# Kernel optimization log

Hardware: AMD Instinct MI355X
Metric: run time of the kernel (lower is better)

## Reference

```python
import jax, jax.numpy as jnp
import numpy as np

B, S, D, H = 2, 2048, 1024, 16
HD = D // H  # head_dim = 64

def setup_inputs() -> dict:
    key = jax.random.key(0)
    ks = jax.random.split(key, 6)
    sc = 0.02
    return {
        "x": jax.random.normal(ks[0], (B, S, D), dtype=jnp.float32),
        "Wq": jax.random.normal(ks[1], (D, D), dtype=jnp.float32) * sc,
        "Wk": jax.random.normal(ks[2], (D, D), dtype=jnp.float32) * sc,
        "Wv": jax.random.normal(ks[3], (D, D), dtype=jnp.float32) * sc,
        "Wo": jax.random.normal(ks[4], (D, D), dtype=jnp.float32) * sc,
        "bo": jnp.zeros((D,), dtype=jnp.float32),
    }

def reference(x, Wq, Wk, Wv, Wo, bo):
    b, s, d = x.shape
    # QKV projections (no bias, qkv_bias=False)
    q = (x @ Wq).reshape(b, s, H, HD).transpose(0, 2, 1, 3)  # [b,h,s,hd]
    k = (x @ Wk).reshape(b, s, H, HD).transpose(0, 2, 1, 3)
    v = (x @ Wv).reshape(b, s, H, HD).transpose(0, 2, 1, 3)
    scores = jnp.einsum("bhqd,bhkd->bhqk", q, k)  # [b,h,s,s]
    causal = jnp.triu(jnp.ones((s, s), dtype=bool), k=1)
    scores = jnp.where(causal, -jnp.inf, scores)
    # NOTE: source divides by keys.shape[-1]**0 / 5 == 1/5 -> scores / 5 (faithful)
    attn = jax.nn.softmax(scores / 5.0, axis=-1)
    ctx = jnp.einsum("bhqk,bhkd->bhqd", attn, v)  # [b,h,s,hd]
    ctx = ctx.transpose(0, 2, 1, 3).reshape(b, s, d)
    return ctx @ Wo + bo
```

## Files before the change

kernel.cpp:

```cpp
#include <hip/hip_runtime.h>
#include <math.h>

#define BB 2
#define SS 2048
#define DD 1024
#define HH 16
#define HD 64
#define MM (BB*SS)

typedef float  f32x4 __attribute__((ext_vector_type(4)));
typedef short  s16x8 __attribute__((ext_vector_type(8)));
typedef unsigned short u16;
typedef u16    u16x4 __attribute__((ext_vector_type(4)));
typedef unsigned int u32;
typedef u32    u32x2 __attribute__((ext_vector_type(2)));
typedef u32    u32x4 __attribute__((ext_vector_type(4)));

static __device__ __forceinline__ u16 f2bf(float f) {
    u32 u = __float_as_uint(f);
    u = (u + 0x7FFFu + ((u >> 16) & 1u)) >> 16;
    return (u16)u;
}

static __device__ __forceinline__ u32 cvtpk_bf16(float lo, float hi) {
    u32 r;
    asm("v_cvt_pk_bf16_f32 %0, %1, %2" : "=v"(r) : "v"(lo), "v"(hi));
    return r;
}

static __device__ __forceinline__ void gload16(const u16* g, void* l) {
    __builtin_amdgcn_global_load_lds((const __attribute__((address_space(1))) u32*)g,
                                     (__attribute__((address_space(3))) u32*)l, 16, 0, 0);
}

__global__ __launch_bounds__(256) void conv_x(const float* __restrict__ in,
                                              u16* __restrict__ outb) {
    int i = blockIdx.x * 256 + threadIdx.x;
    const f32x4* p = (const f32x4*)in;
    f32x4 a = p[i*2], b = p[i*2 + 1];
    u16x4 lo, hi;
    lo[0]=f2bf(a.x); lo[1]=f2bf(a.y); lo[2]=f2bf(a.z); lo[3]=f2bf(a.w);
    hi[0]=f2bf(b.x); hi[1]=f2bf(b.y); hi[2]=f2bf(b.z); hi[3]=f2bf(b.w);
    *(u16x4*)(outb + (size_t)i*8)     = lo;
    *(u16x4*)(outb + (size_t)i*8 + 4) = hi;
}

__global__ __launch_bounds__(256) void conv_wt(const float* __restrict__ W0,
                                               const float* __restrict__ W1,
                                               const float* __restrict__ W2,
                                               const float* __restrict__ W3,
                                               u16* __restrict__ WT) {
    const int z = blockIdx.z;
    const float* W = (z==0) ? W0 : (z==1) ? W1 : (z==2) ? W2 : W3;
    u16* dst = WT + (size_t)z * 1024 * 1024;
    __shared__ u16 tr[64][72];
    const int t = threadIdx.x;
    const int r0 = blockIdx.y * 64, c0 = blockIdx.x * 64;
    #pragma unroll
    for (int u = 0; u < 4; ++u) {
        int idx = u*256 + t;
        int r = idx >> 4, c4 = (idx & 15) * 4;
        f32x4 v = *(const f32x4*)(W + (size_t)(r0 + r)*1024 + c0 + c4);
        tr[c4+0][r] = f2bf(v.x);
        tr[c4+1][r] = f2bf(v.y);
        tr[c4+2][r] = f2bf(v.z);
        tr[c4+3][r] = f2bf(v.w);
    }
    __syncthreads();
    {
        int c = t >> 2, rq = (t & 3) * 16;
        u32x4 v0 = *(const u32x4*)&tr[c][rq];
        u32x4 v1 = *(const u32x4*)&tr[c][rq + 8];
        u16* op = dst + (size_t)(c0 + c)*1024 + r0 + rq;
        *(u32x4*)op       = v0;
        *(u32x4*)(op + 8) = v1;
    }
}

template<int EPI, int NJ>
__global__ __launch_bounds__(256) void mfma_gemm(const u16* __restrict__ A,
                                                 const u16* __restrict__ WT,
                                                 const float* __restrict__ bias,
                                                 u16* __restrict__ Qb,
                                                 u16* __restrict__ Kb,
                                                 u16* __restrict__ Vtb,
                                                 float* __restrict__ outF) {
    constexpr int BN  = NJ * 32;
    constexpr int ASZ = 16384;
    constexpr int BSZ = NJ * 4096;
    __shared__ u32x4 smemv[(2*(ASZ + BSZ))/16];
    char* smem = (char*)smemv;
    char* A0 = smem;
    char* B0 = smem + ASZ;
    char* A1 = smem + ASZ + BSZ;
    char* B1 = smem + 2*ASZ + BSZ;
    const int t   = threadIdx.x;
    const int w   = t >> 6;
    const int l   = t & 63;
    const int c15 = l & 15;
    const int g16 = ((l >> 4) & 3) << 4;
    const int mw  = w >> 1, nw = w & 1;
    const int brow = blockIdx.y * 128;
    const int bcol = blockIdx.x * BN;

    f32x4 acc[4][NJ] = {};

    const u16* Asrc = A  + (size_t)brow * DD;
    const u16* Bsrc = WT + (size_t)bcol * DD;

    auto stage = [&](int k0, char* Ab, char* Bb) {
        #pragma unroll
        for (int u = 0; u < 4; ++u) {
            int idx = u*256 + t;
            int row = idx >> 3;
            int cb  = (idx & 7) << 4;
            int off = (cb ^ ((row & 7) << 4)) >> 1;
            gload16(Asrc + (size_t)row*DD + k0 + off, Ab + ((idx - l) << 4));
        }
        #pragma unroll
        for (int u = 0; u < NJ; ++u) {
            int idx = u*256 + t;
            int row = idx >> 3;
            int cb  = (idx & 7) << 4;
            int off = (cb ^ ((row & 7) << 4)) >> 1;
            gload16(Bsrc + (size_t)row*DD + k0 + off, Bb + ((idx - l) << 4));
        }
    };

    auto compute = [&](char* Ab, char* Bb) {
        s16x8 af[4][2], bf[NJ][2];
        #pragma unroll
        for (int mi = 0; mi < 4; ++mi) {
            int row = mw*64 + mi*16 + c15;
            int sw  = (row & 7) << 4;
            af[mi][0] = *(const s16x8*)(Ab + row*128 + ((g16)      ^ sw));
            af[mi][1] = *(const s16x8*)(Ab + row*128 + ((64 + g16) ^ sw));
        }
        #pragma unroll
        for (int nj = 0; nj < NJ; ++nj) {
            int row = nw*(NJ*16) + nj*16 + c15;
            int sw  = (row & 7) << 4;
            bf[nj][0] = *(const s16x8*)(Bb + row*128 + ((g16)      ^ sw));
            bf[nj][1] = *(const s16x8*)(Bb + row*128 + ((64 + g16) ^ sw));
        }
        #pragma unroll
        for (int c = 0; c < 2; ++c)
            #pragma unroll
            for (int mi = 0; mi < 4; ++mi)
                #pragma unroll
                for (int nj = 0; nj < NJ; ++nj)
                    acc[mi][nj] = __builtin_amdgcn_mfma_f32_16x16x32_bf16(
                        af[mi][c], bf[nj][c], acc[mi][nj], 0, 0, 0);
    };

    stage(0, A0, B0);
    __syncthreads();
    for (int k0 = 0; k0 < DD; k0 += 128) {
        stage(k0 + 64, A1, B1);
        compute(A0, B0);
        __syncthreads();
        if (k0 + 128 < DD) stage(k0 + 128, A0, B0);
        compute(A1, B1);
        __syncthreads();
    }

    if constexpr (EPI == 1) {
        #pragma unroll
        for (int mi = 0; mi < 4; ++mi)
            #pragma unroll
            for (int r = 0; r < 4; ++r) {
                int mg = brow + mw*64 + mi*16 + ((l >> 4) & 3)*4 + r;
                #pragma unroll
                for (int nj = 0; nj < NJ; ++nj) {
                    int nc = bcol + nw*(NJ*16) + nj*16 + c15;
                    outF[(size_t)mg*DD + nc] = acc[mi][nj][r] + bias[nc];
                }
            }
    } else {
        const int wq   = blockIdx.x >> 3;
        const int ncw0 = (blockIdx.x & 7)*128 + nw*64;
        if (wq < 2) {
            u16* dst  = wq ? Kb : Qb;
            float scl = wq ? 1.0f : 0.28853900817779268f;
            #pragma unroll
            for (int mi = 0; mi < 4; ++mi)
                #pragma unroll
                for (int r = 0; r < 4; ++r) {
                    int mg = brow + mw*64 + mi*16 + ((l >> 4) & 3)*4 + r;
                    int b_ = mg >> 11, s_ = mg & (SS-1);
                    #pragma unroll
                    for (int nj = 0; nj < NJ; ++nj) {
                        int nc = ncw0 + nj*16 + c15;
                        int h_ = nc >> 6, d_ = nc & 63;
                        dst[(((size_t)b_*HH + h_)*SS + s_)*HD + d_] =
                            f2bf(acc[mi][nj][r] * scl);
                    }
                }
        } else {
            char* tw = smem + w*8192;
            #pragma unroll
            for (int nj = 0; nj < NJ; ++nj)
                #pragma unroll
                for (int mi = 0; mi < 4; ++mi)
                    #pragma unroll
                    for (int r = 0; r < 4; ++r) {
                        int n = nj*16 + c15;
                        int m = mi*16 + ((l >> 4) & 3)*4 + r;
                        *(u16*)(tw + n*128 + ((m*2) ^ ((n & 7) << 4))) =
                            f2bf(acc[mi][nj][r]);
                    }
            __syncthreads();
            #pragma unroll
            for (int it = 0; it < 8; ++it) {
                int n  = it*8 + (l >> 3);
                int mb = l & 7;
                u32x4 v = *(const u32x4*)(tw + n*128 + ((mb*16) ^ ((n & 7) << 4)));
                int nc = ncw0 + n;
                int h_ = nc >> 6, d_ = nc & 63;
                int mg0 = brow + mw*64;
                int b_ = mg0 >> 11;
                int sb = (mg0 & (SS-1)) + mb*8;
                *(u32x4*)(Vtb + (((size_t)b_*HH + h_)*HD + d_)*SS + sb) = v;
            }
        }
    }
}

__global__ __launch_bounds__(512) void attn_mfma(const u16* __restrict__ Q,
                                                 const u16* __restrict__ K,
                                                 const u16* __restrict__ Vt,
                                                 u16* __restrict__ ctx) {
    __shared__ u32x4 smemv[5120];
    char* smem = (char*)smemv;
    const int pr = blockIdx.x;
    const int h  = blockIdx.y;
    const int b  = blockIdx.z;
    const int t  = threadIdx.x;
    const int w  = t >> 6;
    const int l  = t & 63;
    const int g  = l >> 4;
    const int q15 = l & 15;
    char* Psm = smem + 65536 + w*2048;

    const size_t bh = ((size_t)b*HH + h) * SS;
    const u16* Kg = K  + bh * HD;
    const u16* Vg = Vt + ((size_t)(b*HH + h)) * HD * SS;

    #pragma unroll 1
    for (int half = 0; half < 2; ++half) {
        const int qb = half ? (15 - pr) : pr;
        const u16* Qw = Q + (bh + (size_t)qb*128 + w*16 + q15) * HD;
        s16x8 qf0 = *(const s16x8*)(Qw + g*8);
        s16x8 qf1 = *(const s16x8*)(Qw + 32 + g*8);

        f32x4 acc[4] = {};
        float m = -1e30f, lsum = 0.f;
        const int qg = qb*128 + w*16 + q15;

        u32x4 kreg[2], vreg[2];
        #pragma unroll
        for (int u = 0; u < 2; ++u) {
            int idx = u*512 + t;
            kreg[u] = *(const u32x4*)(Kg + (size_t)(idx >> 3)*HD + (idx & 7)*8);
            vreg[u] = *(const u32x4*)(Vg + (size_t)(idx >> 4)*SS + (idx & 15)*8);
        }
        if (half) __syncthreads();
        #pragma unroll
        for (int u = 0; u < 2; ++u) {
            int idx = u*512 + t;
            int kr = idx >> 3, kc = (idx & 7) << 4;
            *(u32x4*)(smem + kr*128 + (kc ^ ((kr & 7) << 4))) = kreg[u];
            int vr = idx >> 4, vc = (idx & 15) << 4;
            *(u32x4*)(smem + 32768 + vr*256 + (vc ^ ((vr & 7) << 4))) = vreg[u];
        }

        int cur = 0;
        for (int kt = 0; kt <= qb; ++kt) {
            const bool pf = (kt < qb);
            if (pf) {
                #pragma unroll
                for (int u = 0; u < 2; ++u) {
                    int idx = u*512 + t;
                    kreg[u] = *(const u32x4*)(Kg + (size_t)((kt+1)*128 + (idx >> 3))*HD + (idx & 7)*8);
                    vreg[u] = *(const u32x4*)(Vg + (size_t)(idx >> 4)*SS + (kt+1)*128 + (idx & 15)*8);
                }
            }
            __syncthreads();
            char* Kc = smem + (cur << 14);
            char* Vc = smem + 32768 + (cur << 14);

            f32x4 st[8];
            __builtin_amdgcn_s_setprio(1);
            #pragma unroll
            for (int kb = 0; kb < 8; ++kb) {
                f32x4 z = {0.f, 0.f, 0.f, 0.f};
                int row = kb*16 + q15;
                int sw  = (row & 7) << 4;
                s16x8 a0 = *(const s16x8*)(Kc + row*128 + ((g*16)      ^ sw));
                s16x8 a1 = *(const s16x8*)(Kc + row*128 + ((64 + g*16) ^ sw));
                z = __builtin_amdgcn_mfma_f32_16x16x32_bf16(a0, qf0, z, 0, 0, 0);
                z = __builtin_amdgcn_mfma_f32_16x16x32_bf16(a1, qf1, z, 0, 0, 0);
                st[kb] = z;
            }
            __builtin_amdgcn_s_setprio(0);

            if (kt == qb) {
                #pragma unroll
                for (int kb = 0; kb < 8; ++kb)
                    #pragma unroll
                    for (int r = 0; r < 4; ++r) {
                        int key = kt*128 + kb*16 + g*4 + r;
                        if (key > qg) st[kb][r] = -1e30f;
                    }
            }

            float tmax = -1e30f;
            #pragma unroll
            for (int kb = 0; kb < 8; ++kb)
                #pragma unroll
                for (int r = 0; r < 4; ++r) tmax = fmaxf(tmax, st[kb][r]);
            tmax = fmaxf(tmax, __shfl_xor(tmax, 16));
            tmax = fmaxf(tmax, __shfl_xor(tmax, 32));
            if (!__all(tmax - m <= 8.0f)) {
                float mnew = fmaxf(m, tmax);
                float scl  = __builtin_amdgcn_exp2f(m - mnew);
                lsum *= scl;
                #pragma unroll
                for (int r = 0; r < 4; ++r) {
                    float sr = __shfl(scl, g*4 + r);
                    #pragma unroll
                    for (int n = 0; n < 4; ++n) acc[n][r] *= sr;
                }
                m = mnew;
            }
            float ps = 0.f;
            #pragma unroll
            for (int kb = 0; kb < 8; ++kb)
                #pragma unroll
                for (int r = 0; r < 4; ++r) {
                    float p = __builtin_amdgcn_exp2f(st[kb][r] - m);
                    st[kb][r] = p;
                    ps += p;
                }
            ps += __shfl_xor(ps, 16);
            ps += __shfl_xor(ps, 32);
            lsum += ps;

            {
                int swp = (q15 & 7) << 4;
                #pragma unroll
                for (int hf = 0; hf < 2; ++hf) {
                    #pragma unroll
                    for (int kb2 = 0; kb2 < 4; ++kb2) {
                        int kb = hf*4 + kb2;
                        u32x2 pk2;
                        pk2[0] = cvtpk_bf16(st[kb][0], st[kb][1]);
                        pk2[1] = cvtpk_bf16(st[kb][2], st[kb][3]);
                        *(u32x2*)(Psm + q15*128 + ((kb2*32 + g*8) ^ swp)) = pk2;
                    }
                    s16x8 pa[2];
                    #pragma unroll
                    for (int cl = 0; cl < 2; ++cl)
                        pa[cl] = *(const s16x8*)(Psm + q15*128 + ((cl*64 + g*16) ^ swp));
                    __builtin_amdgcn_s_setprio(1);
                    #pragma unroll
                    for (int n = 0; n < 4; ++n) {
                        int row = n*16 + q15;
                        int sw  = (row & 7) << 4;
                        #pragma unroll
                        for (int cl = 0; cl < 2; ++cl) {
                            int c = hf*2 + cl;
                            s16x8 vv = *(const s16x8*)(Vc + row*256 + ((c*64 + g*16) ^ sw));
                            acc[n] = __builtin_amdgcn_mfma_f32_16x16x32_bf16(pa[cl], vv, acc[n], 0, 0, 0);
                        }
                    }
                    __builtin_amdgcn_s_setprio(0);
                }
            }

            if (pf) {
                char* Kn = smem + ((cur ^ 1) << 14);
                char* Vn = smem + 32768 + ((cur ^ 1) << 14);
                #pragma unroll
                for (int u = 0; u < 2; ++u) {
                    int idx = u*512 + t;
                    int kr = idx >> 3, kc = (idx & 7) << 4;
                    *(u32x4*)(Kn + kr*128 + (kc ^ ((kr & 7) << 4))) = kreg[u];
                    int vr = idx >> 4, vc = (idx & 15) << 4;
                    *(u32x4*)(Vn + vr*256 + (vc ^ ((vr & 7) << 4))) = vreg[u];
                }
            }
            cur ^= 1;
        }

        #pragma unroll
        for (int r = 0; r < 4; ++r) {
            float inv = 1.f / __shfl(lsum, g*4 + r);
            int qrow = qb*128 + w*16 + g*4 + r;
            u16* crow = ctx + ((size_t)b*SS + qrow)*DD + h*HD;
            #pragma unroll
            for (int n = 0; n < 4; ++n)
                crow[n*16 + q15] = f2bf(acc[n][r] * inv);
        }
    }
}

extern "C" void kernel_launch(void* const* d_in, const int* in_sizes, int n_in,
                              void* d_out, int out_size, void* d_ws, size_t ws_size,
                              hipStream_t stream) {
    const float* x  = (const float*)d_in[0];
    const float* Wq = (const float*)d_in[1];
    const float* Wk = (const float*)d_in[2];
    const float* Wv = (const float*)d_in[3];
    const float* Wo = (const float*)d_in[4];
    const float* bo = (const float*)d_in[5];
    float* out = (float*)d_out;

    const size_t NELT = (size_t)MM * DD;
    const size_t NW   = (size_t)1024 * 1024;
    u16* wsb  = (u16*)d_ws;
    u16* xb   = wsb;
    u16* WT   = wsb + NELT;
    u16* Qb   = wsb + NELT + 4*NW;
    u16* Kb   = Qb + NELT;
    u16* Vtb  = Kb + NELT;
    u16* Ctxb = Vtb + NELT;
    u16* WTqkv = WT;
    u16* WTo   = WT + 3*NW;

    hipLaunchKernelGGL(conv_x, dim3(2048), dim3(256), 0, stream, x, xb);
    hipLaunchKernelGGL(conv_wt, dim3(16,16,4), dim3(256), 0, stream, Wq, Wk, Wv, Wo, WT);

    hipLaunchKernelGGL((mfma_gemm<0,4>), dim3(24,32), dim3(256), 0, stream,
                       xb, WTqkv, nullptr, Qb, Kb, Vtb, nullptr);

    hipLaunchKernelGGL(attn_mfma, dim3(8,16,2), dim3(512), 0, stream, Qb, Kb, Vtb, Ctxb);

    hipLaunchKernelGGL((mfma_gemm<1,2>), dim3(16,32), dim3(256), 0, stream,
                       Ctxb, WTo, bo, nullptr, nullptr, nullptr, out);
}
```

Before: 100.9 us.

## Process both causal query blocks in one pass sharing K/V tiles

New measurement: 106.0 us. +5.0%, slower.

```diff
diff --git a/kernel.cpp b/kernel.cpp
--- a/kernel.cpp
+++ b/kernel.cpp
@@ -246,162 +246,191 @@
     const u16* Kg = K  + bh * HD;
     const u16* Vg = Vt + ((size_t)(b*HH + h)) * HD * SS;
 
-    #pragma unroll 1
-    for (int half = 0; half < 2; ++half) {
-        const int qb = half ? (15 - pr) : pr;
-        const u16* Qw = Q + (bh + (size_t)qb*128 + w*16 + q15) * HD;
-        s16x8 qf0 = *(const s16x8*)(Qw + g*8);
-        s16x8 qf1 = *(const s16x8*)(Qw + 32 + g*8);
-
-        f32x4 acc[4] = {};
-        float m = -1e30f, lsum = 0.f;
-        const int qg = qb*128 + w*16 + q15;
-
-        u32x4 kreg[2], vreg[2];
-        #pragma unroll
-        for (int u = 0; u < 2; ++u) {
-            int idx = u*512 + t;
-            kreg[u] = *(const u32x4*)(Kg + (size_t)(idx >> 3)*HD + (idx & 7)*8);
-            vreg[u] = *(const u32x4*)(Vg + (size_t)(idx >> 4)*SS + (idx & 15)*8);
-        }
-        if (half) __syncthreads();
-        #pragma unroll
-        for (int u = 0; u < 2; ++u) {
-            int idx = u*512 + t;
-            int kr = idx >> 3, kc = (idx & 7) << 4;
-            *(u32x4*)(smem + kr*128 + (kc ^ ((kr & 7) << 4))) = kreg[u];
-            int vr = idx >> 4, vc = (idx & 15) << 4;
-            *(u32x4*)(smem + 32768 + vr*256 + (vc ^ ((vr & 7) << 4))) = vreg[u];
-        }
-
-        int cur = 0;
-        for (int kt = 0; kt <= qb; ++kt) {
-            const bool pf = (kt < qb);
-            if (pf) {
-                #pragma unroll
-                for (int u = 0; u < 2; ++u) {
-                    int idx = u*512 + t;
-                    kreg[u] = *(const u32x4*)(Kg + (size_t)((kt+1)*128 + (idx >> 3))*HD + (idx & 7)*8);
-                    vreg[u] = *(const u32x4*)(Vg + (size_t)(idx >> 4)*SS + (kt+1)*128 + (idx & 15)*8);
+    const int qbA = pr;
+    const int qbB = 15 - pr;
+    const u16* QwA = Q + (bh + (size_t)qbA*128 + w*16 + q15) * HD;
+    const u16* QwB = Q + (bh + (size_t)qbB*128 + w*16 + q15) * HD;
+    s16x8 qfA0 = *(const s16x8*)(QwA + g*8);
+    s16x8 qfA1 = *(const s16x8*)(QwA + 32 + g*8);
+    s16x8 qfB0 = *(const s16x8*)(QwB + g*8);
+    s16x8 qfB1 = *(const s16x8*)(QwB + 32 + g*8);
+
+    f32x4 accA[4] = {}, accB[4] = {};
+    float mA = -1e30f, lA = 0.f, mB = -1e30f, lB = 0.f;
+    const int qgA = qbA*128 + w*16 + q15;
+    const int qgB = qbB*128 + w*16 + q15;
+
+    auto qk = [&](const char* Kc, s16x8 q0, s16x8 q1, f32x4* st) {
+        __builtin_amdgcn_s_setprio(1);
+        #pragma unroll
+        for (int kb = 0; kb < 8; ++kb) {
+            f32x4 z = {0.f, 0.f, 0.f, 0.f};
+            int row = kb*16 + q15;
+            int sw  = (row & 7) << 4;
+            s16x8 a0 = *(const s16x8*)(Kc + row*128 + ((g*16)      ^ sw));
+            s16x8 a1 = *(const s16x8*)(Kc + row*128 + ((64 + g*16) ^ sw));
+            z = __builtin_amdgcn_mfma_f32_16x16x32_bf16(a0, q0, z, 0, 0, 0);
+            z = __builtin_amdgcn_mfma_f32_16x16x32_bf16(a1, q1, z, 0, 0, 0);
+            st[kb] = z;
+        }
+        __builtin_amdgcn_s_setprio(0);
+    };
+    auto softmax = [&](f32x4* st, f32x4* acc, float& m, float& lsum) {
+        float tmax = -1e30f;
+        #pragma unroll
+        for (int kb = 0; kb < 8; ++kb)
+            #pragma unroll
+            for (int r = 0; r < 4; ++r) tmax = fmaxf(tmax, st[kb][r]);
+        tmax = fmaxf(tmax, __shfl_xor(tmax, 16));
+        tmax = fmaxf(tmax, __shfl_xor(tmax, 32));
+        if (!__all(tmax - m <= 8.0f)) {
+            float mnew = fmaxf(m, tmax);
+            float scl  = __builtin_amdgcn_exp2f(m - mnew);
+            lsum *= scl;
+            #pragma unroll
+            for (int r = 0; r < 4; ++r) {
+                float sr = __shfl(scl, g*4 + r);
+                #pragma unroll
+                for (int n = 0; n < 4; ++n) acc[n][r] *= sr;
+            }
+            m = mnew;
+        }
+        float ps = 0.f;
+        #pragma unroll
+        for (int kb = 0; kb < 8; ++kb)
+            #pragma unroll
+            for (int r = 0; r < 4; ++r) {
+                float p = __builtin_amdgcn_exp2f(st[kb][r] - m);
+                st[kb][r] = p;
+                ps += p;
+            }
+        ps += __shfl_xor(ps, 16);
+        ps += __shfl_xor(ps, 32);
+        lsum += ps;
+    };
+    auto pv = [&](f32x4* st, f32x4* acc, const char* Vc) {
+        int swp = (q15 & 7) << 4;
+        #pragma unroll
+        for (int hf = 0; hf < 2; ++hf) {
+            #pragma unroll
+            for (int kb2 = 0; kb2 < 4; ++kb2) {
+                int kb = hf*4 + kb2;
+                u32x2 pk2;
+                pk2[0] = cvtpk_bf16(st[kb][0], st[kb][1]);
+                pk2[1] = cvtpk_bf16(st[kb][2], st[kb][3]);
+                *(u32x2*)(Psm + q15*128 + ((kb2*32 + g*8) ^ swp)) = pk2;
+            }
+            s16x8 pa[2];
+            #pragma unroll
+            for (int cl = 0; cl < 2; ++cl)
+                pa[cl] = *(const s16x8*)(Psm + q15*128 + ((cl*64 + g*16) ^ swp));
+            __builtin_amdgcn_s_setprio(1);
+            #pragma unroll
+            for (int n = 0; n < 4; ++n) {
+                int row = n*16 + q15;
+                int sw  = (row & 7) << 4;
+                #pragma unroll
+                for (int cl = 0; cl < 2; ++cl) {
+                    int c = hf*2 + cl;
+                    s16x8 vv = *(const s16x8*)(Vc + row*256 + ((c*64 + g*16) ^ sw));
+                    acc[n] = __builtin_amdgcn_mfma_f32_16x16x32_bf16(pa[cl], vv, acc[n], 0, 0, 0);
                 }
             }
-            __syncthreads();
-            char* Kc = smem + (cur << 14);
-            char* Vc = smem + 32768 + (cur << 14);
-
-            f32x4 st[8];
-            __builtin_amdgcn_s_setprio(1);
-            #pragma unroll
-            for (int kb = 0; kb < 8; ++kb) {
-                f32x4 z = {0.f, 0.f, 0.f, 0.f};
-                int row = kb*16 + q15;
-                int sw  = (row & 7) << 4;
-                s16x8 a0 = *(const s16x8*)(Kc + row*128 + ((g*16)      ^ sw));
-                s16x8 a1 = *(const s16x8*)(Kc + row*128 + ((64 + g*16) ^ sw));
-                z = __builtin_amdgcn_mfma_f32_16x16x32_bf16(a0, qf0, z, 0, 0, 0);
-                z = __builtin_amdgcn_mfma_f32_16x16x32_bf16(a1, qf1, z, 0, 0, 0);
-                st[kb] = z;
-            }
             __builtin_amdgcn_s_setprio(0);
-
-            if (kt == qb) {
-                #pragma unroll
-                for (int kb = 0; kb < 8; ++kb)
-                    #pragma unroll
-                    for (int r = 0; r < 4; ++r) {
-                        int key = kt*128 + kb*16 + g*4 + r;
-                        if (key > qg) st[kb][r] = -1e30f;
-                    }
-            }
-
-            float tmax = -1e30f;
+        }
+    };
+
+    u32x4 kreg[2], vreg[2];
+    #pragma unroll
+    for (int u = 0; u < 2; ++u) {
+        int idx = u*512 + t;
+        kreg[u] = *(const u32x4*)(Kg + (size_t)(idx >> 3)*HD + (idx & 7)*8);
+        vreg[u] = *(const u32x4*)(Vg + (size_t)(idx >> 4)*SS + (idx & 15)*8);
+    }
+    #pragma unroll
+    for (int u = 0; u < 2; ++u) {
+        int idx = u*512 + t;
+        int kr = idx >> 3, kc = (idx & 7) << 4;
+        *(u32x4*)(smem + kr*128 + (kc ^ ((kr & 7) << 4))) = kreg[u];
+        int vr = idx >> 4, vc = (idx & 15) << 4;
+        *(u32x4*)(smem + 32768 + vr*256 + (vc ^ ((vr & 7) << 4))) = vreg[u];
+    }
+
+    int cur = 0;
+    for (int kt = 0; kt <= qbB; ++kt) {
+        const bool pf  = (kt < qbB);
+        const bool doA = (kt <= qbA);
+        if (pf) {
+            #pragma unroll
+            for (int u = 0; u < 2; ++u) {
+                int idx = u*512 + t;
+                kreg[u] = *(const u32x4*)(Kg + (size_t)((kt+1)*128 + (idx >> 3))*HD + (idx & 7)*8);
+                vreg[u] = *(const u32x4*)(Vg + (size_t)(idx >> 4)*SS + (kt+1)*128 + (idx & 15)*8);
+            }
+        }
+        __syncthreads();
+        char* Kc = smem + (cur << 14);
+        char* Vc = smem + 32768 + (cur << 14);
+
+        f32x4 stB[8], stA[8];
+        qk(Kc, qfB0, qfB1, stB);
+        if (doA) qk(Kc, qfA0, qfA1, stA);
+
+        if (kt == qbB) {
             #pragma unroll
             for (int kb = 0; kb < 8; ++kb)
                 #pragma unroll
-                for (int r = 0; r < 4; ++r) tmax = fmaxf(tmax, st[kb][r]);
-            tmax = fmaxf(tmax, __shfl_xor(tmax, 16));
-            tmax = fmaxf(tmax, __shfl_xor(tmax, 32));
-            if (!__all(tmax - m <= 8.0f)) {
-                float mnew = fmaxf(m, tmax);
-                float scl  = __builtin_amdgcn_exp2f(m - mnew);
-                lsum *= scl;
-                #pragma unroll
                 for (int r = 0; r < 4; ++r) {
-                    float sr = __shfl(scl, g*4 + r);
-                    #pragma unroll
-                    for (int n = 0; n < 4; ++n) acc[n][r] *= sr;
+                    int key = kt*128 + kb*16 + g*4 + r;
+                    if (key > qgB) stB[kb][r] = -1e30f;
                 }
-                m = mnew;
-            }
-            float ps = 0.f;
+        }
+        if (doA && kt == qbA) {
             #pragma unroll
             for (int kb = 0; kb < 8; ++kb)
                 #pragma unroll
                 for (int r = 0; r < 4; ++r) {
-                    float p = __builtin_amdgcn_exp2f(st[kb][r] - m);
-                    st[kb][r] = p;
-                    ps += p;
+                    int key = kt*128 + kb*16 + g*4 + r;
+                    if (key > qgA) stA[kb][r] = -1e30f;
                 }
-            ps += __shfl_xor(ps, 16);
-            ps += __shfl_xor(ps, 32);
-            lsum += ps;
-
-            {
-                int swp = (q15 & 7) << 4;
-                #pragma unroll
-                for (int hf = 0; hf < 2; ++hf) {
-                    #pragma unroll
-                    for (int kb2 = 0; kb2 < 4; ++kb2) {
-                        int kb = hf*4 + kb2;
-                        u32x2 pk2;
-                        pk2[0] = cvtpk_bf16(st[kb][0], st[kb][1]);
-                        pk2[1] = cvtpk_bf16(st[kb][2], st[kb][3]);
-                        *(u32x2*)(Psm + q15*128 + ((kb2*32 + g*8) ^ swp)) = pk2;
-                    }
-                    s16x8 pa[2];
-                    #pragma unroll
-                    for (int cl = 0; cl < 2; ++cl)
-                        pa[cl] = *(const s16x8*)(Psm + q15*128 + ((cl*64 + g*16) ^ swp));
-                    __builtin_amdgcn_s_setprio(1);
-                    #pragma unroll
-                    for (int n = 0; n < 4; ++n) {
-                        int row = n*16 + q15;
-                        int sw  = (row & 7) << 4;
-                        #pragma unroll
-                        for (int cl = 0; cl < 2; ++cl) {
-                            int c = hf*2 + cl;
-                            s16x8 vv = *(const s16x8*)(Vc + row*256 + ((c*64 + g*16) ^ sw));
-                            acc[n] = __builtin_amdgcn_mfma_f32_16x16x32_bf16(pa[cl], vv, acc[n], 0, 0, 0);
-                        }
-                    }
-                    __builtin_amdgcn_s_setprio(0);
-                }
-            }
-
-            if (pf) {
-                char* Kn = smem + ((cur ^ 1) << 14);
-                char* Vn = smem + 32768 + ((cur ^ 1) << 14);
-                #pragma unroll
-                for (int u = 0; u < 2; ++u) {
-                    int idx = u*512 + t;
-                    int kr = idx >> 3, kc = (idx & 7) << 4;
-                    *(u32x4*)(Kn + kr*128 + (kc ^ ((kr & 7) << 4))) = kreg[u];
-                    int vr = idx >> 4, vc = (idx & 15) << 4;
-                    *(u32x4*)(Vn + vr*256 + (vc ^ ((vr & 7) << 4))) = vreg[u];
-                }
-            }
-            cur ^= 1;
-        }
-
-        #pragma unroll
-        for (int r = 0; r < 4; ++r) {
-            float inv = 1.f / __shfl(lsum, g*4 + r);
-            int qrow = qb*128 + w*16 + g*4 + r;
-            u16* crow = ctx + ((size_t)b*SS + qrow)*DD + h*HD;
-            #pragma unroll
-            for (int n = 0; n < 4; ++n)
-                crow[n*16 + q15] = f2bf(acc[n][r] * inv);
-        }
+        }
+
+        softmax(stB, accB, mB, lB);
+        if (doA) softmax(stA, accA, mA, lA);
+
+        pv(stB, accB, Vc);
+        if (doA) pv(stA, accA, Vc);
+
+        if (pf) {
+            char* Kn = smem + ((cur ^ 1) << 14);
+            char* Vn = smem + 32768 + ((cur ^ 1) << 14);
+            #pragma unroll
+            for (int u = 0; u < 2; ++u) {
+                int idx = u*512 + t;
+                int kr = idx >> 3, kc = (idx & 7) << 4;
+                *(u32x4*)(Kn + kr*128 + (kc ^ ((kr & 7) << 4))) = kreg[u];
+                int vr = idx >> 4, vc = (idx & 15) << 4;
+                *(u32x4*)(Vn + vr*256 + (vc ^ ((vr & 7) << 4))) = vreg[u];
+            }
+        }
+        cur ^= 1;
+    }
+
+    #pragma unroll
+    for (int r = 0; r < 4; ++r) {
+        float invB = 1.f / __shfl(lB, g*4 + r);
+        int qrowB = qbB*128 + w*16 + g*4 + r;
+        u16* crowB = ctx + ((size_t)b*SS + qrowB)*DD + h*HD;
+        #pragma unroll
+        for (int n = 0; n < 4; ++n)
+            crowB[n*16 + q15] = f2bf(accB[n][r] * invB);
+
+        float invA = 1.f / __shfl(lA, g*4 + r);
+        int qrowA = qbA*128 + w*16 + g*4 + r;
+        u16* crowA = ctx + ((size_t)b*SS + qrowA)*DD + h*HD;
+        #pragma unroll
+        for (int n = 0; n < 4; ++n)
+            crowA[n*16 + q15] = f2bf(accA[n][r] * invA);
     }
 }
 
```
